# Optimization experiments

Hardware: AMD Instinct MI355X
Metric: run time of the kernel (lower is better)

Reference implementation:

```python
import jax, jax.numpy as jnp
import numpy as np

MAX = 1e10
H, DK, DV = 16, 64, 64  # heads, key_size, value_size


def setup_inputs() -> dict:
    key = jax.random.key(0)
    ks = jax.random.split(key, 8)
    B, S, D = 2, 2048, 1024
    q = jax.random.normal(ks[0], (B, S, D), dtype=jnp.float32)
    k = jax.random.normal(ks[1], (B, S, D), dtype=jnp.float32)
    v = jax.random.normal(ks[2], (B, S, D), dtype=jnp.float32)
    v_mask = jax.random.randint(ks[3], (B, S), 0, 2, dtype=jnp.int32)
    q_mask = jax.random.randint(ks[4], (B, S), 0, 2, dtype=jnp.int32)
    sc = 1.0 / np.sqrt(D)
    Wq = jax.random.normal(ks[5], (D, H * DK), dtype=jnp.float32) * sc
    Wk = jax.random.normal(ks[6], (D, H * DK), dtype=jnp.float32) * sc
    Wv = jax.random.normal(ks[7], (D, H * DV), dtype=jnp.float32) * sc
    return {"q": q, "k": k, "v": v, "v_mask": v_mask, "q_mask": q_mask,
            "Wq": Wq, "Wk": Wk, "Wv": Wv}


def reference(q, k, v, v_mask, q_mask, Wq, Wk, Wv):
    B, Sq, _ = q.shape
    Sk = k.shape[1]
    # projections -> [B, H, S, d]
    qh = (q @ Wq).reshape(B, Sq, H, DK).transpose(0, 2, 1, 3)
    kh = (k @ Wk).reshape(B, Sk, H, DK).transpose(0, 2, 1, 3)
    vh = (v @ Wv).reshape(B, Sk, H, DV).transpose(0, 2, 1, 3)
    # scores [B, H, Sq, Sk]
    a = jnp.einsum('bhqd,bhkd->bhqk', qh, kh) / np.sqrt(DK).astype(np.float32)
    # additive key-padding mask over key dim
    vm = v_mask.astype(a.dtype)
    a = a - (1.0 - vm)[:, None, None, :] * MAX
    # causal mask (band-part trick)
    causal = jnp.tril(jnp.ones((Sq, Sk), dtype=a.dtype))
    a = a - (1.0 - causal) * MAX
    a = jax.nn.softmax(a, axis=-1)
    out = jnp.einsum('bhqk,bhkd->bqhd', a, vh).reshape(B, Sq, H * DV)
    # multiplicative query-padding mask
    out = out * q_mask.astype(out.dtype)[:, :, None]
    return out
```

## Files before the change

kernel.cpp:

```cpp
#include <hip/hip_runtime.h>
#include <hip/hip_bf16.h>

#define H_    16
#define S_    2048
#define D_    1024
#define MAXV  1e10f

typedef __attribute__((ext_vector_type(8))) short short8;
typedef __attribute__((ext_vector_type(4))) float f32x4;

__device__ __forceinline__ unsigned short f2bf(float f) {
    union { float f; unsigned u; } x; x.f = f;
    unsigned r = x.u + 0x7fffu + ((x.u >> 16) & 1u);
    return (unsigned short)(r >> 16);
}
__device__ __forceinline__ float bf2f(unsigned short h) {
    union { unsigned u; float f; } x; x.u = ((unsigned)h) << 16; return x.f;
}

__global__ __launch_bounds__(256) void scan_kernel(
        const int* __restrict__ vmask, int* __restrict__ cmap,
        int* __restrict__ Jc, int* __restrict__ cumi) {
    int bb = blockIdx.x;
    const int* vm = vmask + (size_t)bb * S_;
    int t = threadIdx.x, lane = t & 63, wave = t >> 6;
    int j0 = t * 8;
    int loc[8], tot = 0;
#pragma unroll
    for (int e = 0; e < 8; e++) { loc[e] = vm[j0 + e] ? 1 : 0; tot += loc[e]; }
    int pre = tot;
#pragma unroll
    for (int d = 1; d < 64; d <<= 1) {
        int x = __shfl_up(pre, d);
        if (lane >= d) pre += x;
    }
    __shared__ int wtot[4];
    if (lane == 63) wtot[wave] = pre;
    __syncthreads();
    int wbase = 0;
    for (int w = 0; w < wave; w++) wbase += wtot[w];
    int run = wbase + pre - tot;
    for (int e = 0; e < 8; e++) {
        int j = j0 + e;
        int before = run;
        run += loc[e];
        cumi[(size_t)bb * S_ + j] = run;
        if (loc[e]) {
            cmap[(size_t)bb * S_ + j] = before;
            Jc[(size_t)bb * S_ + before] = j;
        } else {
            cmap[(size_t)bb * S_ + j] = -1;
        }
    }
    int total = wtot[0] + wtot[1] + wtot[2] + wtot[3];
    for (int c = total + t; c < S_; c += 256) Jc[(size_t)bb * S_ + c] = S_;
}

__global__ __launch_bounds__(256) void wtrans_kernel(
        const float* __restrict__ w0, const float* __restrict__ w1,
        const float* __restrict__ w2, unsigned short* __restrict__ wt) {
    const float* W = blockIdx.z == 0 ? w0 : (blockIdx.z == 1 ? w1 : w2);
    unsigned short* Wt = wt + (size_t)blockIdx.z * (D_ * D_);
    __shared__ float tile[32][33];
    int t = threadIdx.x;
    int k0 = blockIdx.y * 32, n0 = blockIdx.x * 32;
    int r = t >> 3, c4 = (t & 7) * 4;
    float4 v = *(const float4*)&W[(size_t)(k0 + r) * D_ + n0 + c4];
    tile[r][c4 + 0] = v.x; tile[r][c4 + 1] = v.y;
    tile[r][c4 + 2] = v.z; tile[r][c4 + 3] = v.w;
    __syncthreads();
    ushort4 o;
    o.x = f2bf(tile[c4 + 0][r]); o.y = f2bf(tile[c4 + 1][r]);
    o.z = f2bf(tile[c4 + 2][r]); o.w = f2bf(tile[c4 + 3][r]);
    *(ushort4*)&Wt[(size_t)(n0 + r) * D_ + k0 + c4] = o;
}

__global__ __launch_bounds__(256) void conv_kernel(
        const float* __restrict__ q, const float* __restrict__ k,
        const float* __restrict__ v, unsigned short* __restrict__ abf) {
    int z = blockIdx.y;
    const float* src = z == 0 ? q : (z == 1 ? k : v);
    unsigned short* dst = abf + (size_t)z * (4096ull * 1024);
    size_t i = ((size_t)blockIdx.x * 256 + threadIdx.x) * 8;
    float4 f1 = *(const float4*)&src[i];
    float4 f2 = *(const float4*)&src[i + 4];
    short8 o;
    o[0] = (short)f2bf(f1.x); o[1] = (short)f2bf(f1.y);
    o[2] = (short)f2bf(f1.z); o[3] = (short)f2bf(f1.w);
    o[4] = (short)f2bf(f2.x); o[5] = (short)f2bf(f2.y);
    o[6] = (short)f2bf(f2.z); o[7] = (short)f2bf(f2.w);
    *(short8*)&dst[i] = o;
}

template <bool PRE>
__global__ __launch_bounds__(256) void proj_kernel(
        const float* __restrict__ q, const float* __restrict__ k,
        const float* __restrict__ v, const unsigned short* __restrict__ abf,
        const unsigned short* __restrict__ wt, const int* __restrict__ cmap,
        unsigned short* __restrict__ Qh, unsigned short* __restrict__ Kc,
        unsigned short* __restrict__ Vtc) {
    int z = blockIdx.z;
    const float* Af = z == 0 ? q : (z == 1 ? k : v);
    const unsigned short* Ab = abf + (size_t)z * (4096ull * 1024);
    const unsigned short* Bt = wt + (size_t)z * (D_ * D_);
    int m0 = blockIdx.y * 128;
    int n0 = blockIdx.x * 128;
    __shared__ __align__(16) unsigned short As[128][72];
    __shared__ __align__(16) unsigned short Bs[128][72];
    int t = threadIdx.x;
    int wave = t >> 6, lane = t & 63, lg = lane >> 4, lr = lane & 15;
    int wr = (wave >> 1) * 64, wc = (wave & 1) * 64;
    f32x4 acc[4][4];
#pragma unroll
    for (int mi = 0; mi < 4; mi++)
#pragma unroll
        for (int ni = 0; ni < 4; ni++) acc[mi][ni] = (f32x4){0.f, 0.f, 0.f, 0.f};

    int srow = t >> 3, scol = (t & 7) * 8;
    short8 aa[4], bb2[4];
    float4 af_[4][2];
#pragma unroll
    for (int i = 0; i < 4; i++) {
        int row = i * 32 + srow;
        if (PRE) {
            aa[i] = *(const short8*)&Ab[(size_t)(m0 + row) * D_ + scol];
        } else {
            af_[i][0] = *(const float4*)&Af[(size_t)(m0 + row) * D_ + scol];
            af_[i][1] = *(const float4*)&Af[(size_t)(m0 + row) * D_ + scol + 4];
        }
        bb2[i] = *(const short8*)&Bt[(size_t)(n0 + row) * D_ + scol];
    }
    for (int kt = 0; kt < D_ / 64; ++kt) {
#pragma unroll
        for (int i = 0; i < 4; i++) {
            int row = i * 32 + srow;
            if (PRE) {
                *(short8*)&As[row][scol] = aa[i];
            } else {
                short8 o;
                o[0] = (short)f2bf(af_[i][0].x); o[1] = (short)f2bf(af_[i][0].y);
                o[2] = (short)f2bf(af_[i][0].z); o[3] = (short)f2bf(af_[i][0].w);
                o[4] = (short)f2bf(af_[i][1].x); o[5] = (short)f2bf(af_[i][1].y);
                o[6] = (short)f2bf(af_[i][1].z); o[7] = (short)f2bf(af_[i][1].w);
                *(short8*)&As[row][scol] = o;
            }
            *(short8*)&Bs[row][scol] = bb2[i];
        }
        __syncthreads();
        if (kt + 1 < D_ / 64) {
            int kk0 = (kt + 1) * 64;
#pragma unroll
            for (int i = 0; i < 4; i++) {
                int row = i * 32 + srow;
                if (PRE) {
                    aa[i] = *(const short8*)&Ab[(size_t)(m0 + row) * D_ + kk0 + scol];
                } else {
                    af_[i][0] = *(const float4*)&Af[(size_t)(m0 + row) * D_ + kk0 + scol];
                    af_[i][1] = *(const float4*)&Af[(size_t)(m0 + row) * D_ + kk0 + scol + 4];
                }
                bb2[i] = *(const short8*)&Bt[(size_t)(n0 + row) * D_ + kk0 + scol];
            }
        }
        short8 af[4][2], bq[4][2];
#pragma unroll
        for (int mi = 0; mi < 4; mi++)
#pragma unroll
            for (int kh = 0; kh < 2; kh++)
                af[mi][kh] = *(const short8*)&As[wr + mi * 16 + lr][kh * 32 + lg * 8];
#pragma unroll
        for (int ni = 0; ni < 4; ni++)
#pragma unroll
            for (int kh = 0; kh < 2; kh++)
                bq[ni][kh] = *(const short8*)&Bs[wc + ni * 16 + lr][kh * 32 + lg * 8];
        __builtin_amdgcn_s_setprio(1);
#pragma unroll
        for (int kh = 0; kh < 2; kh++)
#pragma unroll
            for (int mi = 0; mi < 4; mi++)
#pragma unroll
                for (int ni = 0; ni < 4; ni++)
                    acc[mi][ni] = __builtin_amdgcn_mfma_f32_16x16x32_bf16(
                        af[mi][kh], bq[ni][kh], acc[mi][ni], 0, 0, 0);
        __builtin_amdgcn_s_setprio(0);
        __syncthreads();
    }
    if (z == 0) {
#pragma unroll
        for (int mi = 0; mi < 4; mi++) {
#pragma unroll
            for (int ni = 0; ni < 4; ni++) {
                int col = n0 + wc + ni * 16 + lr;
                int hh = col >> 6, dk = col & 63;
#pragma unroll
                for (int rr = 0; rr < 4; rr++) {
                    int m = m0 + wr + mi * 16 + lg * 4 + rr;
                    int bb = m >> 11, s = m & (S_ - 1);
                    Qh[(((size_t)(bb * H_ + hh)) * S_ + s) * 64 + dk] =
                        f2bf(acc[mi][ni][rr]);
                }
            }
        }
    } else {
        int cm_[4][4], bb_[4][4];
#pragma unroll
        for (int mi = 0; mi < 4; mi++)
#pragma unroll
            for (int rr = 0; rr < 4; rr++) {
                int m = m0 + wr + mi * 16 + lg * 4 + rr;
                int bb = m >> 11, s = m & (S_ - 1);
                bb_[mi][rr] = bb;
                cm_[mi][rr] = cmap[(size_t)bb * S_ + s];
            }
#pragma unroll
        for (int mi = 0; mi < 4; mi++) {
#pragma unroll
            for (int ni = 0; ni < 4; ni++) {
                int col = n0 + wc + ni * 16 + lr;
                int hh = col >> 6, dd = col & 63;
#pragma unroll
                for (int rr = 0; rr < 4; rr++) {
                    int c = cm_[mi][rr];
                    if (c < 0) continue;
                    int bb = bb_[mi][rr];
                    if (z == 1)
                        Kc[(((size_t)(bb * H_ + hh)) * S_ + c) * 64 + dd] =
                            f2bf(acc[mi][ni][rr]);
                    else
                        Vtc[(((size_t)(bb * H_ + hh)) * 64 + dd) * S_ + c] =
                            f2bf(acc[mi][ni][rr]);
                }
            }
        }
    }
}

__global__ __launch_bounds__(256) void attn_kernel(
        const unsigned short* __restrict__ Qh, const unsigned short* __restrict__ Kc,
        const unsigned short* __restrict__ Vtc, const int* __restrict__ Jc,
        const int* __restrict__ cumi, const int* __restrict__ qmask,
        float* __restrict__ out) {
    int fid = blockIdx.x;
    int xcd = fid & 7, slot = fid >> 3;
    int qt = 31 - (slot >> 2);
    int g = xcd + 8 * (slot & 3);
    int hh = g & 15, bb = g >> 4;
    const unsigned short* Qp = Qh + ((size_t)(bb * H_ + hh)) * S_ * 64;
    const unsigned short* Kp = Kc + ((size_t)(bb * H_ + hh)) * S_ * 64;
    const unsigned short* Vp = Vtc + ((size_t)(bb * H_ + hh)) * 64 * S_;
    const int* Jb = Jc + (size_t)bb * S_;
    int t = threadIdx.x, wave = t >> 6, lane = t & 63, lg = lane >> 4, lr = lane & 15;
    __shared__ __align__(16) unsigned short Ks[64 * 64];
    __shared__ __align__(16) unsigned short Vs[64 * 64];
    __shared__ __align__(16) unsigned short Pl[4][16][72];

    int q0 = qt * 64 + wave * 16;
    int nc = cumi[(size_t)bb * S_ + qt * 64 + 63];
    int nt = (nc + 63) >> 6;
    short8 qf[2];
#pragma unroll
    for (int kh = 0; kh < 2; kh++)
        qf[kh] = *(const short8*)&Qp[(size_t)(q0 + lr) * 64 + kh * 32 + lg * 8];
    f32x4 oacc[4];
#pragma unroll
    for (int ni = 0; ni < 4; ni++) oacc[ni] = (f32x4){0.f, 0.f, 0.f, 0.f};
    float m_run[4], l_run[4];
    int qrow[4];
#pragma unroll
    for (int rr = 0; rr < 4; rr++) {
        m_run[rr] = -__builtin_inff(); l_run[rr] = 0.f;
        qrow[rr] = q0 + lg * 4 + rr;
    }
    int soff[2], srw[2], scsw[2];
#pragma unroll
    for (int i = 0; i < 2; i++) {
        soff[i] = i * 4096 + t * 16;
        srw[i] = soff[i] >> 7;
        scsw[i] = (soff[i] & 127) ^ ((srw[i] & 7) << 4);
    }
    short8 kreg[2], vreg[2];
    if (nt > 0) {
#pragma unroll
        for (int i = 0; i < 2; i++) {
            kreg[i] = *(const short8*)((const char*)Kp + (size_t)srw[i] * 128 + scsw[i]);
            vreg[i] = *(const short8*)((const char*)Vp + (size_t)srw[i] * 4096 + scsw[i]);
        }
    }

    for (int kt = 0; kt < nt; ++kt) {
        int kv0 = kt * 64;
#pragma unroll
        for (int i = 0; i < 2; i++) {
            *(short8*)((char*)Ks + soff[i]) = kreg[i];
            *(short8*)((char*)Vs + soff[i]) = vreg[i];
        }
        __syncthreads();
        if (kt + 1 < nt) {
            int kv0n = (kt + 1) * 64;
#pragma unroll
            for (int i = 0; i < 2; i++) {
                kreg[i] = *(const short8*)((const char*)Kp + (size_t)(kv0n + srw[i]) * 128 + scsw[i]);
                vreg[i] = *(const short8*)((const char*)Vp + (size_t)srw[i] * 4096 + kv0n * 2 + scsw[i]);
            }
        }
        f32x4 sacc[4];
#pragma unroll
        for (int ni = 0; ni < 4; ni++) sacc[ni] = (f32x4){0.f, 0.f, 0.f, 0.f};
        __builtin_amdgcn_s_setprio(1);
#pragma unroll
        for (int ni = 0; ni < 4; ni++) {
            int row = ni * 16 + lr;
#pragma unroll
            for (int kh = 0; kh < 2; kh++) {
                int cb = (kh * 64 + lg * 16) ^ ((row & 7) << 4);
                short8 kf = *(const short8*)((const char*)Ks + row * 128 + cb);
                sacc[ni] = __builtin_amdgcn_mfma_f32_16x16x32_bf16(qf[kh], kf, sacc[ni], 0, 0, 0);
            }
        }
        __builtin_amdgcn_s_setprio(0);
        float sv[4][4];
#pragma unroll
        for (int ni = 0; ni < 4; ni++) {
            int jo = Jb[kv0 + ni * 16 + lr];
#pragma unroll
            for (int rr = 0; rr < 4; rr++) {
                float s = sacc[ni][rr] * 0.125f;
                if (jo > qrow[rr]) s -= MAXV;
                sv[ni][rr] = s;
            }
        }
        float scl[4];
#pragma unroll
        for (int rr = 0; rr < 4; rr++) {
            float a = fmaxf(fmaxf(sv[0][rr], sv[1][rr]), fmaxf(sv[2][rr], sv[3][rr]));
#pragma unroll
            for (int d = 1; d < 16; d <<= 1) a = fmaxf(a, __shfl_xor(a, d));
            float mn = fmaxf(m_run[rr], a);
            scl[rr] = __expf(m_run[rr] - mn);
            m_run[rr] = mn;
        }
        float pw[4][4], ps[4];
#pragma unroll
        for (int rr = 0; rr < 4; rr++) ps[rr] = 0.f;
#pragma unroll
        for (int ni = 0; ni < 4; ni++)
#pragma unroll
            for (int rr = 0; rr < 4; rr++) {
                pw[ni][rr] = __expf(sv[ni][rr] - m_run[rr]);
                ps[rr] += pw[ni][rr];
            }
#pragma unroll
        for (int rr = 0; rr < 4; rr++) {
#pragma unroll
            for (int d = 1; d < 16; d <<= 1) ps[rr] += __shfl_xor(ps[rr], d);
            l_run[rr] = l_run[rr] * scl[rr] + ps[rr];
        }
#pragma unroll
        for (int ni = 0; ni < 4; ni++)
#pragma unroll
            for (int rr = 0; rr < 4; rr++) oacc[ni][rr] *= scl[rr];
#pragma unroll
        for (int ni = 0; ni < 4; ni++)
#pragma unroll
            for (int rr = 0; rr < 4; rr++)
                Pl[wave][lg * 4 + rr][ni * 16 + lr] = f2bf(pw[ni][rr]);
        short8 pa[2];
#pragma unroll
        for (int kh = 0; kh < 2; kh++)
            pa[kh] = *(const short8*)&Pl[wave][lr][kh * 32 + lg * 8];
        __builtin_amdgcn_s_setprio(1);
#pragma unroll
        for (int ni = 0; ni < 4; ni++) {
            int rowd = ni * 16 + lr;
#pragma unroll
            for (int kh = 0; kh < 2; kh++) {
                int cb = (kh * 64 + lg * 16) ^ ((rowd & 7) << 4);
                short8 vf = *(const short8*)((const char*)Vs + rowd * 128 + cb);
                oacc[ni] = __builtin_amdgcn_mfma_f32_16x16x32_bf16(pa[kh], vf, oacc[ni], 0, 0, 0);
            }
        }
        __builtin_amdgcn_s_setprio(0);
        __syncthreads();
    }
#pragma unroll
    for (int rr = 0; rr < 4; rr++) {
        int qm = qmask[bb * S_ + qrow[rr]];
        float f = (qm != 0 && l_run[rr] > 0.f) ? (float)qm / l_run[rr] : 0.f;
#pragma unroll
        for (int ni = 0; ni < 4; ni++)
            out[((size_t)(bb * S_ + qrow[rr])) * D_ + hh * 64 + ni * 16 + lr] =
                oacc[ni][rr] * f;
    }
}

__global__ __launch_bounds__(256) void fixup_kernel(
        const int* __restrict__ qmask, const float* __restrict__ v,
        const unsigned short* __restrict__ wt, const unsigned short* __restrict__ Vtc,
        const int* __restrict__ Jc, const int* __restrict__ cumi,
        float* __restrict__ out) {
    int bb = blockIdx.y;
    int p0 = blockIdx.x * 16;
    int t = threadIdx.x;
    int pl = t >> 4, jl = t & 15;
    int d = Jc[(size_t)bb * S_];
    if (d == 0) return;
    int ccount = cumi[(size_t)bb * S_ + S_ - 1];
    int p = p0 + pl;
    int hh = p >> 6, dv = p & 63;
    const unsigned short* vrow = Vtc + ((size_t)(bb * H_ + hh) * 64 + dv) * S_;
    float suf = 0.f;
    for (int c = jl; c < ccount; c += 16) suf += bf2f(vrow[c]);
#pragma unroll
    for (int dd = 1; dd < 16; dd <<= 1) suf += __shfl_xor(suf, dd);
    const unsigned short* wcol = wt + 2ull * D_ * D_ + (size_t)p * D_;
    float pre = 0.f;
    for (int r = 0; r < d; ++r) {
        const float* vr = v + ((size_t)bb * S_ + r) * D_;
        float acc = 0.f;
        for (int kk = jl * 64; kk < jl * 64 + 64; kk += 8) {
            float4 a1 = *(const float4*)&vr[kk];
            float4 a2 = *(const float4*)&vr[kk + 4];
            acc += a1.x * bf2f(wcol[kk + 0]) + a1.y * bf2f(wcol[kk + 1]) +
                   a1.z * bf2f(wcol[kk + 2]) + a1.w * bf2f(wcol[kk + 3]) +
                   a2.x * bf2f(wcol[kk + 4]) + a2.y * bf2f(wcol[kk + 5]) +
                   a2.z * bf2f(wcol[kk + 6]) + a2.w * bf2f(wcol[kk + 7]);
        }
#pragma unroll
        for (int dd = 1; dd < 16; dd <<= 1) acc += __shfl_xor(acc, dd);
        pre += acc;
        if (jl == 0 && qmask[(size_t)bb * S_ + r] != 0)
            out[((size_t)(bb * S_ + r)) * D_ + p] =
                (pre + suf) / (float)(r + 1 + ccount);
    }
}

extern "C" void kernel_launch(void* const* d_in, const int* in_sizes, int n_in,
                              void* d_out, int out_size, void* d_ws, size_t ws_size,
                              hipStream_t stream) {
    const float* q  = (const float*)d_in[0];
    const float* k  = (const float*)d_in[1];
    const float* v  = (const float*)d_in[2];
    const int* vmask = (const int*)d_in[3];
    const int* qmask = (const int*)d_in[4];
    const float* Wq = (const float*)d_in[5];
    const float* Wk = (const float*)d_in[6];
    const float* Wv = (const float*)d_in[7];
    float* out = (float*)d_out;

    char* ws = (char*)d_ws;
    const size_t MB = 1024ull * 1024;
    int* cmap = (int*)ws;
    int* Jc   = (int*)(ws + 16 * 1024);
    int* cumi = (int*)(ws + 32 * 1024);
    unsigned short* Wt  = (unsigned short*)(ws + 64 * 1024);
    unsigned short* Qh  = (unsigned short*)(ws + 64 * 1024 + 6 * MB);
    unsigned short* Kc  = (unsigned short*)(ws + 64 * 1024 + 14 * MB);
    unsigned short* Vtc = (unsigned short*)(ws + 64 * 1024 + 22 * MB);
    unsigned short* Abf = (unsigned short*)(ws + 64 * 1024 + 30 * MB);
    bool pre = ws_size >= 64 * 1024 + 54 * MB;

    scan_kernel<<<dim3(2), 256, 0, stream>>>(vmask, cmap, Jc, cumi);
    wtrans_kernel<<<dim3(32, 32, 3), 256, 0, stream>>>(Wq, Wk, Wv, Wt);
    if (pre) {
        conv_kernel<<<dim3(2048, 3), 256, 0, stream>>>(q, k, v, Abf);
        proj_kernel<true><<<dim3(8, 32, 3), 256, 0, stream>>>(
            q, k, v, Abf, Wt, cmap, Qh, Kc, Vtc);
    } else {
        proj_kernel<false><<<dim3(8, 32, 3), 256, 0, stream>>>(
            q, k, v, Abf, Wt, cmap, Qh, Kc, Vtc);
    }
    attn_kernel<<<dim3(1024), 256, 0, stream>>>(Qh, Kc, Vtc, Jc, cumi, qmask, out);
    fixup_kernel<<<dim3(64, 2), 256, 0, stream>>>(qmask, v, Wt, Vtc, Jc, cumi, out);
}
```

Before: 214.7 us.

## Process two query sub-tiles per attention block and drop separate bf16 conversion pass

The attention kernel now handles 128 query rows per block, as two 64-row sub-tiles per wave, so each staged K/V tile in shared memory is reused twice. The grid shrinks from 1024 to 512 blocks. The separate conv_kernel pre-pass that converted q/k/v to bf16 is removed, and the projection kernel always converts fp32 inputs inline. The K/V reuse cuts global loads and barrier count, but doubles per-wave register state, which may hurt occupancy. The coarser causal tiles also leave less parallelism and more masked work per block.

```diff
diff --git a/kernel.cpp b/kernel.cpp
--- a/kernel.cpp
+++ b/kernel.cpp
@@ -75,33 +75,14 @@
     *(ushort4*)&Wt[(size_t)(n0 + r) * D_ + k0 + c4] = o;
 }
 
-__global__ __launch_bounds__(256) void conv_kernel(
-        const float* __restrict__ q, const float* __restrict__ k,
-        const float* __restrict__ v, unsigned short* __restrict__ abf) {
-    int z = blockIdx.y;
-    const float* src = z == 0 ? q : (z == 1 ? k : v);
-    unsigned short* dst = abf + (size_t)z * (4096ull * 1024);
-    size_t i = ((size_t)blockIdx.x * 256 + threadIdx.x) * 8;
-    float4 f1 = *(const float4*)&src[i];
-    float4 f2 = *(const float4*)&src[i + 4];
-    short8 o;
-    o[0] = (short)f2bf(f1.x); o[1] = (short)f2bf(f1.y);
-    o[2] = (short)f2bf(f1.z); o[3] = (short)f2bf(f1.w);
-    o[4] = (short)f2bf(f2.x); o[5] = (short)f2bf(f2.y);
-    o[6] = (short)f2bf(f2.z); o[7] = (short)f2bf(f2.w);
-    *(short8*)&dst[i] = o;
-}
-
-template <bool PRE>
 __global__ __launch_bounds__(256) void proj_kernel(
         const float* __restrict__ q, const float* __restrict__ k,
-        const float* __restrict__ v, const unsigned short* __restrict__ abf,
-        const unsigned short* __restrict__ wt, const int* __restrict__ cmap,
+        const float* __restrict__ v, const unsigned short* __restrict__ wt,
+        const int* __restrict__ cmap,
         unsigned short* __restrict__ Qh, unsigned short* __restrict__ Kc,
         unsigned short* __restrict__ Vtc) {
     int z = blockIdx.z;
     const float* Af = z == 0 ? q : (z == 1 ? k : v);
-    const unsigned short* Ab = abf + (size_t)z * (4096ull * 1024);
     const unsigned short* Bt = wt + (size_t)z * (D_ * D_);
     int m0 = blockIdx.y * 128;
     int n0 = blockIdx.x * 128;
@@ -117,33 +98,25 @@
         for (int ni = 0; ni < 4; ni++) acc[mi][ni] = (f32x4){0.f, 0.f, 0.f, 0.f};
 
     int srow = t >> 3, scol = (t & 7) * 8;
-    short8 aa[4], bb2[4];
+    short8 bb2[4];
     float4 af_[4][2];
 #pragma unroll
     for (int i = 0; i < 4; i++) {
         int row = i * 32 + srow;
-        if (PRE) {
-            aa[i] = *(const short8*)&Ab[(size_t)(m0 + row) * D_ + scol];
-        } else {
-            af_[i][0] = *(const float4*)&Af[(size_t)(m0 + row) * D_ + scol];
-            af_[i][1] = *(const float4*)&Af[(size_t)(m0 + row) * D_ + scol + 4];
-        }
+        af_[i][0] = *(const float4*)&Af[(size_t)(m0 + row) * D_ + scol];
+        af_[i][1] = *(const float4*)&Af[(size_t)(m0 + row) * D_ + scol + 4];
         bb2[i] = *(const short8*)&Bt[(size_t)(n0 + row) * D_ + scol];
     }
     for (int kt = 0; kt < D_ / 64; ++kt) {
 #pragma unroll
         for (int i = 0; i < 4; i++) {
             int row = i * 32 + srow;
-            if (PRE) {
-                *(short8*)&As[row][scol] = aa[i];
-            } else {
-                short8 o;
-                o[0] = (short)f2bf(af_[i][0].x); o[1] = (short)f2bf(af_[i][0].y);
-                o[2] = (short)f2bf(af_[i][0].z); o[3] = (short)f2bf(af_[i][0].w);
-                o[4] = (short)f2bf(af_[i][1].x); o[5] = (short)f2bf(af_[i][1].y);
-                o[6] = (short)f2bf(af_[i][1].z); o[7] = (short)f2bf(af_[i][1].w);
-                *(short8*)&As[row][scol] = o;
-            }
+            short8 o;
+            o[0] = (short)f2bf(af_[i][0].x); o[1] = (short)f2bf(af_[i][0].y);
+            o[2] = (short)f2bf(af_[i][0].z); o[3] = (short)f2bf(af_[i][0].w);
+            o[4] = (short)f2bf(af_[i][1].x); o[5] = (short)f2bf(af_[i][1].y);
+            o[6] = (short)f2bf(af_[i][1].z); o[7] = (short)f2bf(af_[i][1].w);
+            *(short8*)&As[row][scol] = o;
             *(short8*)&Bs[row][scol] = bb2[i];
         }
         __syncthreads();
@@ -152,12 +125,8 @@
 #pragma unroll
             for (int i = 0; i < 4; i++) {
                 int row = i * 32 + srow;
-                if (PRE) {
-                    aa[i] = *(const short8*)&Ab[(size_t)(m0 + row) * D_ + kk0 + scol];
-                } else {
-                    af_[i][0] = *(const float4*)&Af[(size_t)(m0 + row) * D_ + kk0 + scol];
-                    af_[i][1] = *(const float4*)&Af[(size_t)(m0 + row) * D_ + kk0 + scol + 4];
-                }
+                af_[i][0] = *(const float4*)&Af[(size_t)(m0 + row) * D_ + kk0 + scol];
+                af_[i][1] = *(const float4*)&Af[(size_t)(m0 + row) * D_ + kk0 + scol + 4];
                 bb2[i] = *(const short8*)&Bt[(size_t)(n0 + row) * D_ + kk0 + scol];
             }
         }
@@ -241,7 +210,7 @@
         float* __restrict__ out) {
     int fid = blockIdx.x;
     int xcd = fid & 7, slot = fid >> 3;
-    int qt = 31 - (slot >> 2);
+    int pp = 15 - (slot >> 2);
     int g = xcd + 8 * (slot & 3);
     int hh = g & 15, bb = g >> 4;
     const unsigned short* Qp = Qh + ((size_t)(bb * H_ + hh)) * S_ * 64;
@@ -253,22 +222,26 @@
     __shared__ __align__(16) unsigned short Vs[64 * 64];
     __shared__ __align__(16) unsigned short Pl[4][16][72];
 
-    int q0 = qt * 64 + wave * 16;
-    int nc = cumi[(size_t)bb * S_ + qt * 64 + 63];
+    int qb0 = pp * 128;
+    int nc = cumi[(size_t)bb * S_ + qb0 + 127];
     int nt = (nc + 63) >> 6;
-    short8 qf[2];
-#pragma unroll
-    for (int kh = 0; kh < 2; kh++)
-        qf[kh] = *(const short8*)&Qp[(size_t)(q0 + lr) * 64 + kh * 32 + lg * 8];
-    f32x4 oacc[4];
-#pragma unroll
-    for (int ni = 0; ni < 4; ni++) oacc[ni] = (f32x4){0.f, 0.f, 0.f, 0.f};
-    float m_run[4], l_run[4];
-    int qrow[4];
-#pragma unroll
-    for (int rr = 0; rr < 4; rr++) {
-        m_run[rr] = -__builtin_inff(); l_run[rr] = 0.f;
-        qrow[rr] = q0 + lg * 4 + rr;
+    short8 qf[2][2];
+    f32x4 oacc[2][4];
+    float m_run[2][4], l_run[2][4];
+    int qrow[2][4];
+#pragma unroll
+    for (int ss = 0; ss < 2; ss++) {
+        int q0 = qb0 + ss * 64 + wave * 16;
+#pragma unroll
+        for (int kh = 0; kh < 2; kh++)
+            qf[ss][kh] = *(const short8*)&Qp[(size_t)(q0 + lr) * 64 + kh * 32 + lg * 8];
+#pragma unroll
+        for (int ni = 0; ni < 4; ni++) oacc[ss][ni] = (f32x4){0.f, 0.f, 0.f, 0.f};
+#pragma unroll
+        for (int rr = 0; rr < 4; rr++) {
+            m_run[ss][rr] = -__builtin_inff(); l_run[ss][rr] = 0.f;
+            qrow[ss][rr] = q0 + lg * 4 + rr;
+        }
     }
     int soff[2], srw[2], scsw[2];
 #pragma unroll
@@ -302,94 +275,101 @@
                 vreg[i] = *(const short8*)((const char*)Vp + (size_t)srw[i] * 4096 + kv0n * 2 + scsw[i]);
             }
         }
-        f32x4 sacc[4];
-#pragma unroll
-        for (int ni = 0; ni < 4; ni++) sacc[ni] = (f32x4){0.f, 0.f, 0.f, 0.f};
-        __builtin_amdgcn_s_setprio(1);
-#pragma unroll
-        for (int ni = 0; ni < 4; ni++) {
-            int row = ni * 16 + lr;
-#pragma unroll
-            for (int kh = 0; kh < 2; kh++) {
-                int cb = (kh * 64 + lg * 16) ^ ((row & 7) << 4);
-                short8 kf = *(const short8*)((const char*)Ks + row * 128 + cb);
-                sacc[ni] = __builtin_amdgcn_mfma_f32_16x16x32_bf16(qf[kh], kf, sacc[ni], 0, 0, 0);
-            }
-        }
-        __builtin_amdgcn_s_setprio(0);
-        float sv[4][4];
-#pragma unroll
-        for (int ni = 0; ni < 4; ni++) {
-            int jo = Jb[kv0 + ni * 16 + lr];
+        int jo[4];
+#pragma unroll
+        for (int ni = 0; ni < 4; ni++) jo[ni] = Jb[kv0 + ni * 16 + lr];
+
+#pragma unroll
+        for (int ss = 0; ss < 2; ss++) {
+            f32x4 sacc[4];
+#pragma unroll
+            for (int ni = 0; ni < 4; ni++) sacc[ni] = (f32x4){0.f, 0.f, 0.f, 0.f};
+            __builtin_amdgcn_s_setprio(1);
+#pragma unroll
+            for (int ni = 0; ni < 4; ni++) {
+                int row = ni * 16 + lr;
+#pragma unroll
+                for (int kh = 0; kh < 2; kh++) {
+                    int cb = (kh * 64 + lg * 16) ^ ((row & 7) << 4);
+                    short8 kf = *(const short8*)((const char*)Ks + row * 128 + cb);
+                    sacc[ni] = __builtin_amdgcn_mfma_f32_16x16x32_bf16(qf[ss][kh], kf, sacc[ni], 0, 0, 0);
+                }
+            }
+            __builtin_amdgcn_s_setprio(0);
+            float sv[4][4];
+#pragma unroll
+            for (int ni = 0; ni < 4; ni++)
+#pragma unroll
+                for (int rr = 0; rr < 4; rr++) {
+                    float s = sacc[ni][rr] * 0.125f;
+                    if (jo[ni] > qrow[ss][rr]) s -= MAXV;
+                    sv[ni][rr] = s;
+                }
+            float scl[4];
 #pragma unroll
             for (int rr = 0; rr < 4; rr++) {
-                float s = sacc[ni][rr] * 0.125f;
-                if (jo > qrow[rr]) s -= MAXV;
-                sv[ni][rr] = s;
-            }
-        }
-        float scl[4];
+                float a = fmaxf(fmaxf(sv[0][rr], sv[1][rr]), fmaxf(sv[2][rr], sv[3][rr]));
+#pragma unroll
+                for (int d = 1; d < 16; d <<= 1) a = fmaxf(a, __shfl_xor(a, d));
+                float mn = fmaxf(m_run[ss][rr], a);
+                scl[rr] = __expf(m_run[ss][rr] - mn);
+                m_run[ss][rr] = mn;
+            }
+            float pw[4][4], ps[4];
+#pragma unroll
+            for (int rr = 0; rr < 4; rr++) ps[rr] = 0.f;
+#pragma unroll
+            for (int ni = 0; ni < 4; ni++)
+#pragma unroll
+                for (int rr = 0; rr < 4; rr++) {
+                    pw[ni][rr] = __expf(sv[ni][rr] - m_run[ss][rr]);
+                    ps[rr] += pw[ni][rr];
+                }
+#pragma unroll
+            for (int rr = 0; rr < 4; rr++) {
+#pragma unroll
+                for (int d = 1; d < 16; d <<= 1) ps[rr] += __shfl_xor(ps[rr], d);
+                l_run[ss][rr] = l_run[ss][rr] * scl[rr] + ps[rr];
+            }
+#pragma unroll
+            for (int ni = 0; ni < 4; ni++)
+#pragma unroll
+                for (int rr = 0; rr < 4; rr++) oacc[ss][ni][rr] *= scl[rr];
+#pragma unroll
+            for (int ni = 0; ni < 4; ni++)
+#pragma unroll
+                for (int rr = 0; rr < 4; rr++)
+                    Pl[wave][lg * 4 + rr][ni * 16 + lr] = f2bf(pw[ni][rr]);
+            short8 pa[2];
+#pragma unroll
+            for (int kh = 0; kh < 2; kh++)
+                pa[kh] = *(const short8*)&Pl[wave][lr][kh * 32 + lg * 8];
+            __builtin_amdgcn_s_setprio(1);
+#pragma unroll
+            for (int ni = 0; ni < 4; ni++) {
+                int rowd = ni * 16 + lr;
+#pragma unroll
+                for (int kh = 0; kh < 2; kh++) {
+                    int cb = (kh * 64 + lg * 16) ^ ((rowd & 7) << 4);
+                    short8 vf = *(const short8*)((const char*)Vs + rowd * 128 + cb);
+                    oacc[ss][ni] = __builtin_amdgcn_mfma_f32_16x16x32_bf16(pa[kh], vf, oacc[ss][ni], 0, 0, 0);
+                }
+            }
+            __builtin_amdgcn_s_setprio(0);
+        }
+        __syncthreads();
+    }
+#pragma unroll
+    for (int ss = 0; ss < 2; ss++)
 #pragma unroll
         for (int rr = 0; rr < 4; rr++) {
-            float a = fmaxf(fmaxf(sv[0][rr], sv[1][rr]), fmaxf(sv[2][rr], sv[3][rr]));
-#pragma unroll
-            for (int d = 1; d < 16; d <<= 1) a = fmaxf(a, __shfl_xor(a, d));
-            float mn = fmaxf(m_run[rr], a);
-            scl[rr] = __expf(m_run[rr] - mn);
-            m_run[rr] = mn;
-        }
-        float pw[4][4], ps[4];
-#pragma unroll
-        for (int rr = 0; rr < 4; rr++) ps[rr] = 0.f;
-#pragma unroll
-        for (int ni = 0; ni < 4; ni++)
-#pragma unroll
-            for (int rr = 0; rr < 4; rr++) {
-                pw[ni][rr] = __expf(sv[ni][rr] - m_run[rr]);
-                ps[rr] += pw[ni][rr];
-            }
-#pragma unroll
-        for (int rr = 0; rr < 4; rr++) {
-#pragma unroll
-            for (int d = 1; d < 16; d <<= 1) ps[rr] += __shfl_xor(ps[rr], d);
-            l_run[rr] = l_run[rr] * scl[rr] + ps[rr];
-        }
-#pragma unroll
-        for (int ni = 0; ni < 4; ni++)
-#pragma unroll
-            for (int rr = 0; rr < 4; rr++) oacc[ni][rr] *= scl[rr];
-#pragma unroll
-        for (int ni = 0; ni < 4; ni++)
-#pragma unroll
-            for (int rr = 0; rr < 4; rr++)
-                Pl[wave][lg * 4 + rr][ni * 16 + lr] = f2bf(pw[ni][rr]);
-        short8 pa[2];
-#pragma unroll
-        for (int kh = 0; kh < 2; kh++)
-            pa[kh] = *(const short8*)&Pl[wave][lr][kh * 32 + lg * 8];
-        __builtin_amdgcn_s_setprio(1);
-#pragma unroll
-        for (int ni = 0; ni < 4; ni++) {
-            int rowd = ni * 16 + lr;
-#pragma unroll
-            for (int kh = 0; kh < 2; kh++) {
-                int cb = (kh * 64 + lg * 16) ^ ((rowd & 7) << 4);
-                short8 vf = *(const short8*)((const char*)Vs + rowd * 128 + cb);
-                oacc[ni] = __builtin_amdgcn_mfma_f32_16x16x32_bf16(pa[kh], vf, oacc[ni], 0, 0, 0);
-            }
-        }
-        __builtin_amdgcn_s_setprio(0);
-        __syncthreads();
-    }
-#pragma unroll
-    for (int rr = 0; rr < 4; rr++) {
-        int qm = qmask[bb * S_ + qrow[rr]];
-        float f = (qm != 0 && l_run[rr] > 0.f) ? (float)qm / l_run[rr] : 0.f;
-#pragma unroll
-        for (int ni = 0; ni < 4; ni++)
-            out[((size_t)(bb * S_ + qrow[rr])) * D_ + hh * 64 + ni * 16 + lr] =
-                oacc[ni][rr] * f;
-    }
+            int qm = qmask[bb * S_ + qrow[ss][rr]];
+            float f = (qm != 0 && l_run[ss][rr] > 0.f) ? (float)qm / l_run[ss][rr] : 0.f;
+#pragma unroll
+            for (int ni = 0; ni < 4; ni++)
+                out[((size_t)(bb * S_ + qrow[ss][rr])) * D_ + hh * 64 + ni * 16 + lr] =
+                    oacc[ss][ni][rr] * f;
+        }
 }
 
 __global__ __launch_bounds__(256) void fixup_kernel(
@@ -455,19 +435,10 @@
     unsigned short* Qh  = (unsigned short*)(ws + 64 * 1024 + 6 * MB);
     unsigned short* Kc  = (unsigned short*)(ws + 64 * 1024 + 14 * MB);
     unsigned short* Vtc = (unsigned short*)(ws + 64 * 1024 + 22 * MB);
-    unsigned short* Abf = (unsigned short*)(ws + 64 * 1024 + 30 * MB);
-    bool pre = ws_size >= 64 * 1024 + 54 * MB;
 
     scan_kernel<<<dim3(2), 256, 0, stream>>>(vmask, cmap, Jc, cumi);
     wtrans_kernel<<<dim3(32, 32, 3), 256, 0, stream>>>(Wq, Wk, Wv, Wt);
-    if (pre) {
-        conv_kernel<<<dim3(2048, 3), 256, 0, stream>>>(q, k, v, Abf);
-        proj_kernel<true><<<dim3(8, 32, 3), 256, 0, stream>>>(
-            q, k, v, Abf, Wt, cmap, Qh, Kc, Vtc);
-    } else {
-        proj_kernel<false><<<dim3(8, 32, 3), 256, 0, stream>>>(
-            q, k, v, Abf, Wt, cmap, Qh, Kc, Vtc);
-    }
-    attn_kernel<<<dim3(1024), 256, 0, stream>>>(Qh, Kc, Vtc, Jc, cumi, qmask, out);
+    proj_kernel<<<dim3(8, 32, 3), 256, 0, stream>>>(q, k, v, Wt, cmap, Qh, Kc, Vtc);
+    attn_kernel<<<dim3(512), 256, 0, stream>>>(Qh, Kc, Vtc, Jc, cumi, qmask, out);
     fixup_kernel<<<dim3(64, 2), 256, 0, stream>>>(qmask, v, Wt, Vtc, Jc, cumi, out);
 }
```

Result: slower. 240.3 us (+11.9%).
